# Performance work log

Measured on AMD Instinct MI355X. Metric: run time of the kernel, lower is better.

Reference implementation:

```python
import jax, jax.numpy as jnp
import numpy as np

B, S1, S2, H1, H2, HID = 8, 512, 512, 128, 128, 128

def setup_inputs() -> dict:
    key = jax.random.key(0)
    ks = jax.random.split(key, 8)
    return {
        "query": jax.random.normal(ks[0], (B, S1, H1), jnp.float32),
        "key": jax.random.normal(ks[1], (B, S2, H2), jnp.float32),
        "value": jax.random.normal(ks[2], (B, S2, H2), jnp.float32),
        "q_mask": jax.random.randint(ks[3], (B, S1), 0, 2, jnp.int32),
        "k_mask": jax.random.randint(ks[4], (B, S2), 0, 2, jnp.int32),
        # init_weights: Linear weight ~ N(0, 0.01), bias = 0
        "W1": jax.random.normal(ks[5], (HID, H1 + H2), jnp.float32) * 0.01,
        "b1": jnp.zeros((HID,), jnp.float32),
        "W2": jax.random.normal(ks[6], (1, HID), jnp.float32) * 0.01,
        "b2": jnp.zeros((1,), jnp.float32),
    }

def reference(query, key, value, q_mask, k_mask, W1, b1, W2, b2):
    h1 = query.shape[-1]
    # Linear on concat([q,k]) == q @ W1[:, :h1].T + k @ W1[:, h1:].T + b1
    qp = jnp.einsum('bsd,hd->bsh', query, W1[:, :h1]) + b1   # [B,S1,HID]
    kp = jnp.einsum('btd,hd->bth', key, W1[:, h1:])          # [B,S2,HID]
    h = jax.nn.relu(qp[:, :, None, :] + kp[:, None, :, :])   # [B,S1,S2,HID]
    s = jnp.einsum('bsth,h->bst', h, W2[0]) + b2[0]          # [B,S1,S2]
    mask = (q_mask[:, :, None] * k_mask[:, None, :]) > 0     # [B,S1,S2]
    A = jnp.where(mask, jnp.exp(s), 0.0)                     # masked_fill(-inf).exp()
    A_sum = jnp.clip(jnp.sum(A, axis=-1, keepdims=True), 2e-15, None)
    attn = A / A_sum
    return jnp.einsum('bst,btd->bsd', attn, value)           # [B,S1,H2]
```

## Files before the change

kernel.cpp:

```cpp
#include <hip/hip_runtime.h>

#define S 512
#define H 128
#define NROW 4096
#define TI 8

typedef _Float16 h2v __attribute__((ext_vector_type(2)));
#define BCH(x) __builtin_bit_cast(h2v, (x))

__global__ __launch_bounds__(256) void proj_kernel(
    const float* __restrict__ query, const float* __restrict__ key,
    const float* __restrict__ W1, const float* __restrict__ b1,
    const float* __restrict__ W2,
    unsigned* __restrict__ qph, unsigned* __restrict__ kph,
    unsigned* __restrict__ w2h)
{
  __shared__ float w1t[128][130];
  const int bid = blockIdx.x;
  const bool isq = bid < 128;
  const float* __restrict__ src = isq ? query : key;
  const int rbase = (isq ? bid : bid - 128) * 32;
  const int off = isq ? 0 : 128;
  const int tid = threadIdx.x;

  if (bid == 0 && tid < 64) {
    h2v p;
    p.x = (_Float16)W2[2 * tid];
    p.y = (_Float16)W2[2 * tid + 1];
    w2h[tid] = __builtin_bit_cast(unsigned, p);
  }

  for (int idx = tid; idx < 128 * 32; idx += 256) {
    const int d4 = idx & 31, h = idx >> 5;
    const float4 v = *(const float4*)(W1 + h * 256 + off + d4 * 4);
    w1t[d4 * 4 + 0][h] = v.x;
    w1t[d4 * 4 + 1][h] = v.y;
    w1t[d4 * 4 + 2][h] = v.z;
    w1t[d4 * 4 + 3][h] = v.w;
  }
  __syncthreads();

  const int w = __builtin_amdgcn_readfirstlane(tid >> 6);
  const int lane = tid & 63;
  const int r0 = rbase + w * 8;

  float acc[8][2];
  float2 bv = make_float2(0.f, 0.f);
  if (isq) bv = *(const float2*)(b1 + 2 * lane);
  #pragma unroll
  for (int r = 0; r < 8; r++) { acc[r][0] = bv.x; acc[r][1] = bv.y; }

  for (int dc = 0; dc < 128; dc += 8) {
    float qs[8][8];
    #pragma unroll
    for (int r = 0; r < 8; r++) {
      const float* sp = src + (size_t)(r0 + r) * H + dc;
      #pragma unroll
      for (int u = 0; u < 8; u++) qs[r][u] = sp[u];
    }
    #pragma unroll
    for (int dd = 0; dd < 8; dd++) {
      const float2 wv = *(const float2*)&w1t[dc + dd][2 * lane];
      #pragma unroll
      for (int r = 0; r < 8; r++) {
        acc[r][0] = __builtin_fmaf(qs[r][dd], wv.x, acc[r][0]);
        acc[r][1] = __builtin_fmaf(qs[r][dd], wv.y, acc[r][1]);
      }
    }
  }
  unsigned* __restrict__ dst = isq ? qph : kph;
  #pragma unroll
  for (int r = 0; r < 8; r++) {
    h2v p;
    p.x = (_Float16)acc[r][0];
    p.y = (_Float16)acc[r][1];
    dst[(size_t)(r0 + r) * 64 + lane] = __builtin_bit_cast(unsigned, p);
  }
}

__global__ __launch_bounds__(512) void attn_kernel(
    const unsigned* __restrict__ qph, const unsigned* __restrict__ kph,
    const unsigned* __restrict__ w2h, const float* __restrict__ value,
    const int* __restrict__ q_mask, const int* __restrict__ k_mask,
    const float* __restrict__ b2, float* __restrict__ out)
{
  union __align__(16) SMU {
    float aT[8][64][12];
    float numk[8][TI][128];
  };
  __shared__ SMU sm;
  __shared__ float denk[8][TI];

  const int it = blockIdx.x;
  const int r0 = it * TI;
  const int b = r0 >> 9;
  const int tid = threadIdx.x;
  const int w = __builtin_amdgcn_readfirstlane(tid >> 6);
  const int lane = tid & 63;
  const int jl = (w << 6) + lane;
  const int jg = (b << 9) + jl;
  const int km = k_mask[jg];
  const unsigned* __restrict__ kprow = kph + (size_t)jg * 64;
  const float b2v = b2[0];
  const h2v hz = {};

  float s[TI];
  #pragma unroll
  for (int i = 0; i < TI; i++) s[i] = 0.f;

  for (int hc = 0; hc < 64; hc += 16) {
    h2v kr[16];
    {
      const uint4* k4 = (const uint4*)(kprow + hc);
      const uint4 a0 = k4[0], a1 = k4[1], a2 = k4[2], a3 = k4[3];
      kr[0]  = BCH(a0.x); kr[1]  = BCH(a0.y); kr[2]  = BCH(a0.z); kr[3]  = BCH(a0.w);
      kr[4]  = BCH(a1.x); kr[5]  = BCH(a1.y); kr[6]  = BCH(a1.z); kr[7]  = BCH(a1.w);
      kr[8]  = BCH(a2.x); kr[9]  = BCH(a2.y); kr[10] = BCH(a2.z); kr[11] = BCH(a2.w);
      kr[12] = BCH(a3.x); kr[13] = BCH(a3.y); kr[14] = BCH(a3.z); kr[15] = BCH(a3.w);
    }
    h2v w2c[16];
    #pragma unroll
    for (int u = 0; u < 16; u++) w2c[u] = BCH(w2h[hc + u]);

    #pragma unroll
    for (int i = 0; i < TI; i++) {
      const unsigned* __restrict__ qrow =
          qph + (size_t)(r0 + i) * 64 + hc;
      unsigned qu[16];
      #pragma unroll
      for (int u = 0; u < 16; u++) qu[u] = qrow[u];
      #pragma unroll
      for (int u = 0; u < 16; u++) {
        h2v t = BCH(qu[u]) + kr[u];
        t = __builtin_elementwise_max(t, hz);
        s[i] = __builtin_amdgcn_fdot2(t, w2c[u], s[i], false);
      }
    }
  }

  float a[TI];
  #pragma unroll
  for (int i = 0; i < TI; i++) {
    const int qm = q_mask[r0 + i];
    a[i] = (km > 0 && qm > 0) ? __expf(s[i] + b2v) : 0.f;
  }
  #pragma unroll
  for (int i = 0; i < TI; i++) {
    float d = a[i];
    #pragma unroll
    for (int m = 32; m >= 1; m >>= 1) d += __shfl_xor(d, m, 64);
    if (lane == 0) denk[w][i] = d;
  }
  *(float4*)&sm.aT[w][lane][0] = make_float4(a[0], a[1], a[2], a[3]);
  *(float4*)&sm.aT[w][lane][4] = make_float4(a[4], a[5], a[6], a[7]);
  __syncthreads();

  const int lj = lane >> 5, lh = lane & 31;
  float nr[TI][4];
  #pragma unroll
  for (int i = 0; i < TI; i++) { nr[i][0]=0.f; nr[i][1]=0.f; nr[i][2]=0.f; nr[i][3]=0.f; }
  const float* __restrict__ vbase =
      value + ((size_t)b * S + (w << 6)) * H;

  for (int js = 0; js < 32; js++) {
    const int j = js * 2 + lj;
    const float4 vv = *(const float4*)(vbase + (size_t)j * H + lh * 4);
    float av[TI];
    { const float4 t0 = *(const float4*)&sm.aT[w][j][0];
      const float4 t1 = *(const float4*)&sm.aT[w][j][4];
      av[0]=t0.x; av[1]=t0.y; av[2]=t0.z; av[3]=t0.w;
      av[4]=t1.x; av[5]=t1.y; av[6]=t1.z; av[7]=t1.w; }
    #pragma unroll
    for (int i = 0; i < TI; i++) {
      nr[i][0] = __builtin_fmaf(av[i], vv.x, nr[i][0]);
      nr[i][1] = __builtin_fmaf(av[i], vv.y, nr[i][1]);
      nr[i][2] = __builtin_fmaf(av[i], vv.z, nr[i][2]);
      nr[i][3] = __builtin_fmaf(av[i], vv.w, nr[i][3]);
    }
  }
  #pragma unroll
  for (int i = 0; i < TI; i++) {
    #pragma unroll
    for (int k = 0; k < 4; k++) nr[i][k] += __shfl_xor(nr[i][k], 32, 64);
  }

  __syncthreads();
  if (lane < 32) {
    #pragma unroll
    for (int i = 0; i < TI; i++)
      *(float4*)&sm.numk[w][i][lane * 4] =
          make_float4(nr[i][0], nr[i][1], nr[i][2], nr[i][3]);
  }
  __syncthreads();

  const int ii = tid >> 6;
  const int h0 = (tid & 63) * 2;
  float nx = 0.f, ny = 0.f, d = 0.f;
  #pragma unroll
  for (int ww = 0; ww < 8; ww++) {
    const float2 t = *(const float2*)&sm.numk[ww][ii][h0];
    nx += t.x; ny += t.y;
    d += denk[ww][ii];
  }
  const float inv = 1.f / fmaxf(d, 2e-15f);
  *(float2*)(out + (size_t)(r0 + ii) * H + h0) = make_float2(nx * inv, ny * inv);
}

extern "C" void kernel_launch(void* const* d_in, const int* in_sizes, int n_in,
                              void* d_out, int out_size, void* d_ws, size_t ws_size,
                              hipStream_t stream)
{
  (void)in_sizes; (void)n_in; (void)out_size; (void)ws_size;
  const float* query  = (const float*)d_in[0];
  const float* key    = (const float*)d_in[1];
  const float* value  = (const float*)d_in[2];
  const int*   q_mask = (const int*)d_in[3];
  const int*   k_mask = (const int*)d_in[4];
  const float* W1     = (const float*)d_in[5];
  const float* b1     = (const float*)d_in[6];
  const float* W2     = (const float*)d_in[7];
  const float* b2     = (const float*)d_in[8];
  float* out = (float*)d_out;

  unsigned* ws  = (unsigned*)d_ws;
  unsigned* qph = ws;
  unsigned* kph = ws + (size_t)NROW * 64;
  unsigned* w2h = kph + (size_t)NROW * 64;

  proj_kernel<<<256, 256, 0, stream>>>(query, key, W1, b1, W2, qph, kph, w2h);
  attn_kernel<<<512, 512, 0, stream>>>(qph, kph, w2h, value, q_mask, k_mask,
                                       b2, out);
}
```

Before: 111.9 us.

## Split work into more blocks for both kernels to raise occupancy and parallelism

The projection kernel now uses 1024 blocks of 8 rows each and stages W1 in two 64-wide halves, which cuts shared memory and raises block count. The attention kernel processes 4 query rows per block instead of 8, launches 1024 blocks with a 6-wave occupancy hint, and reorders block indices so neighbouring blocks cover different batches. It also pads the numerator staging buffer and writes scalar outputs. The intent is to fill the GPU's compute units better. The cost is that K rows and value rows are reloaded twice as often per query row, and W1 is re-staged per block.

```diff
diff --git a/kernel.cpp b/kernel.cpp
--- a/kernel.cpp
+++ b/kernel.cpp
@@ -3,7 +3,7 @@
 #define S 512
 #define H 128
 #define NROW 4096
-#define TI 8
+#define TI 4
 
 typedef _Float16 h2v __attribute__((ext_vector_type(2)));
 #define BCH(x) __builtin_bit_cast(h2v, (x))
@@ -15,13 +15,13 @@
     unsigned* __restrict__ qph, unsigned* __restrict__ kph,
     unsigned* __restrict__ w2h)
 {
-  __shared__ float w1t[128][130];
+  __shared__ float w1t[64][130];
   const int bid = blockIdx.x;
-  const bool isq = bid < 128;
+  const int tid = threadIdx.x;
+  const bool isq = bid < 512;
   const float* __restrict__ src = isq ? query : key;
-  const int rbase = (isq ? bid : bid - 128) * 32;
+  const int rbase = (isq ? bid : bid - 512) * 8;
   const int off = isq ? 0 : 128;
-  const int tid = threadIdx.x;
 
   if (bid == 0 && tid < 64) {
     h2v p;
@@ -30,47 +30,51 @@
     w2h[tid] = __builtin_bit_cast(unsigned, p);
   }
 
-  for (int idx = tid; idx < 128 * 32; idx += 256) {
-    const int d4 = idx & 31, h = idx >> 5;
-    const float4 v = *(const float4*)(W1 + h * 256 + off + d4 * 4);
-    w1t[d4 * 4 + 0][h] = v.x;
-    w1t[d4 * 4 + 1][h] = v.y;
-    w1t[d4 * 4 + 2][h] = v.z;
-    w1t[d4 * 4 + 3][h] = v.w;
-  }
-  __syncthreads();
-
   const int w = __builtin_amdgcn_readfirstlane(tid >> 6);
   const int lane = tid & 63;
-  const int r0 = rbase + w * 8;
-
-  float acc[8][2];
+  const int r0 = rbase + w * 2;
+
+  float acc[2][2];
   float2 bv = make_float2(0.f, 0.f);
   if (isq) bv = *(const float2*)(b1 + 2 * lane);
-  #pragma unroll
-  for (int r = 0; r < 8; r++) { acc[r][0] = bv.x; acc[r][1] = bv.y; }
-
-  for (int dc = 0; dc < 128; dc += 8) {
-    float qs[8][8];
-    #pragma unroll
-    for (int r = 0; r < 8; r++) {
-      const float* sp = src + (size_t)(r0 + r) * H + dc;
-      #pragma unroll
-      for (int u = 0; u < 8; u++) qs[r][u] = sp[u];
-    }
-    #pragma unroll
-    for (int dd = 0; dd < 8; dd++) {
-      const float2 wv = *(const float2*)&w1t[dc + dd][2 * lane];
-      #pragma unroll
-      for (int r = 0; r < 8; r++) {
-        acc[r][0] = __builtin_fmaf(qs[r][dd], wv.x, acc[r][0]);
-        acc[r][1] = __builtin_fmaf(qs[r][dd], wv.y, acc[r][1]);
+  acc[0][0] = bv.x; acc[0][1] = bv.y;
+  acc[1][0] = bv.x; acc[1][1] = bv.y;
+
+  for (int p = 0; p < 2; p++) {
+    for (int idx = tid; idx < 128 * 16; idx += 256) {
+      const int d4 = idx & 15, h = idx >> 4;
+      const float4 v = *(const float4*)(W1 + h * 256 + off + p * 64 + d4 * 4);
+      w1t[d4 * 4 + 0][h] = v.x;
+      w1t[d4 * 4 + 1][h] = v.y;
+      w1t[d4 * 4 + 2][h] = v.z;
+      w1t[d4 * 4 + 3][h] = v.w;
+    }
+    __syncthreads();
+
+    for (int dc = 0; dc < 64; dc += 8) {
+      float qs[2][8];
+      #pragma unroll
+      for (int r = 0; r < 2; r++) {
+        const float* sp = src + (size_t)(r0 + r) * H + p * 64 + dc;
+        #pragma unroll
+        for (int u = 0; u < 8; u++) qs[r][u] = sp[u];
       }
-    }
-  }
+      #pragma unroll
+      for (int dd = 0; dd < 8; dd++) {
+        const float2 wv = *(const float2*)&w1t[dc + dd][2 * lane];
+        #pragma unroll
+        for (int r = 0; r < 2; r++) {
+          acc[r][0] = __builtin_fmaf(qs[r][dd], wv.x, acc[r][0]);
+          acc[r][1] = __builtin_fmaf(qs[r][dd], wv.y, acc[r][1]);
+        }
+      }
+    }
+    __syncthreads();
+  }
+
   unsigned* __restrict__ dst = isq ? qph : kph;
   #pragma unroll
-  for (int r = 0; r < 8; r++) {
+  for (int r = 0; r < 2; r++) {
     h2v p;
     p.x = (_Float16)acc[r][0];
     p.y = (_Float16)acc[r][1];
@@ -78,7 +82,7 @@
   }
 }
 
-__global__ __launch_bounds__(512) void attn_kernel(
+__global__ __launch_bounds__(512, 6) void attn_kernel(
     const unsigned* __restrict__ qph, const unsigned* __restrict__ kph,
     const unsigned* __restrict__ w2h, const float* __restrict__ value,
     const int* __restrict__ q_mask, const int* __restrict__ k_mask,
@@ -86,12 +90,13 @@
 {
   union __align__(16) SMU {
     float aT[8][64][12];
-    float numk[8][TI][128];
+    float numk[8][TI][132];
   };
   __shared__ SMU sm;
   __shared__ float denk[8][TI];
 
-  const int it = blockIdx.x;
+  const int bid = blockIdx.x;
+  const int it = (bid & 7) * 128 + (bid >> 3);
   const int r0 = it * TI;
   const int b = r0 >> 9;
   const int tid = threadIdx.x;
@@ -152,7 +157,6 @@
     if (lane == 0) denk[w][i] = d;
   }
   *(float4*)&sm.aT[w][lane][0] = make_float4(a[0], a[1], a[2], a[3]);
-  *(float4*)&sm.aT[w][lane][4] = make_float4(a[4], a[5], a[6], a[7]);
   __syncthreads();
 
   const int lj = lane >> 5, lh = lane & 31;
@@ -162,14 +166,13 @@
   const float* __restrict__ vbase =
       value + ((size_t)b * S + (w << 6)) * H;
 
+  #pragma unroll 4
   for (int js = 0; js < 32; js++) {
     const int j = js * 2 + lj;
     const float4 vv = *(const float4*)(vbase + (size_t)j * H + lh * 4);
     float av[TI];
     { const float4 t0 = *(const float4*)&sm.aT[w][j][0];
-      const float4 t1 = *(const float4*)&sm.aT[w][j][4];
-      av[0]=t0.x; av[1]=t0.y; av[2]=t0.z; av[3]=t0.w;
-      av[4]=t1.x; av[5]=t1.y; av[6]=t1.z; av[7]=t1.w; }
+      av[0]=t0.x; av[1]=t0.y; av[2]=t0.z; av[3]=t0.w; }
     #pragma unroll
     for (int i = 0; i < TI; i++) {
       nr[i][0] = __builtin_fmaf(av[i], vv.x, nr[i][0]);
@@ -193,17 +196,16 @@
   }
   __syncthreads();
 
-  const int ii = tid >> 6;
-  const int h0 = (tid & 63) * 2;
-  float nx = 0.f, ny = 0.f, d = 0.f;
+  const int ii = tid >> 7;
+  const int h0 = tid & 127;
+  float nx = 0.f, d = 0.f;
   #pragma unroll
   for (int ww = 0; ww < 8; ww++) {
-    const float2 t = *(const float2*)&sm.numk[ww][ii][h0];
-    nx += t.x; ny += t.y;
+    nx += sm.numk[ww][ii][h0];
     d += denk[ww][ii];
   }
   const float inv = 1.f / fmaxf(d, 2e-15f);
-  *(float2*)(out + (size_t)(r0 + ii) * H + h0) = make_float2(nx * inv, ny * inv);
+  out[(size_t)(r0 + ii) * H + h0] = nx * inv;
 }
 
 extern "C" void kernel_launch(void* const* d_in, const int* in_sizes, int n_in,
@@ -227,7 +229,7 @@
   unsigned* kph = ws + (size_t)NROW * 64;
   unsigned* w2h = kph + (size_t)NROW * 64;
 
-  proj_kernel<<<256, 256, 0, stream>>>(query, key, W1, b1, W2, qph, kph, w2h);
-  attn_kernel<<<512, 512, 0, stream>>>(qph, kph, w2h, value, q_mask, k_mask,
-                                       b2, out);
+  proj_kernel<<<1024, 256, 0, stream>>>(query, key, W1, b1, W2, qph, kph, w2h);
+  attn_kernel<<<1024, 512, 0, stream>>>(qph, kph, w2h, value, q_mask, k_mask,
+                                        b2, out);
 }
```

Result: slower. 115.0 us (+2.8%).
